# Optimization experiments

Hardware: AMD Instinct MI355X
Metric: run time of the kernel (lower is better)

## Reference

```python
import jax, jax.numpy as jnp
import numpy as np
from jax.ops import segment_sum

N = 20000; IN = 256; HID = 256; Z = 64; DEC_H = 64; E = 120000; NEG = 5
BETA = 1.0; LN_EPS = 1e-5; TAU_MIN = 1e-4


def setup_inputs() -> dict:
    rng = np.random.default_rng(0)
    a = rng.integers(0, N, E)
    b = (a + 1 + rng.integers(0, N - 1, E)) % N  # guarantees a != b
    lo, hi = np.minimum(a, b), np.maximum(a, b)
    pos_edge = jnp.asarray(np.stack([lo, hi]), dtype=jnp.int32)          # [2,E], i<j single copy
    edge_index = jnp.asarray(np.stack([np.concatenate([lo, hi]),
                                       np.concatenate([hi, lo])]), dtype=jnp.int32)  # [2,2E] undirected
    neg_edge = jnp.asarray(rng.integers(0, N, (2, NEG * E)), dtype=jnp.int32)
    ks = jax.random.split(jax.random.key(0), 12)
    p = lambda i, shape, s=0.02: (jax.random.normal(ks[i], shape, jnp.float32) * s)
    return dict(
        x=p(0, (N, IN), 1.0), eps=p(1, (N, Z), 1.0),
        edge_index=edge_index, pos_edge=pos_edge, neg_edge=neg_edge,
        W1=p(2, (IN, HID)), b1=jnp.zeros((HID,), jnp.float32),
        g1=jnp.ones((HID,), jnp.float32), bt1=jnp.zeros((HID,), jnp.float32),
        Wmu=p(3, (HID, Z)), bmu=jnp.zeros((Z,), jnp.float32),
        Wlv=p(4, (HID, Z)), blv=jnp.zeros((Z,), jnp.float32),
        Wd1=p(5, (Z, Z)), bd1=jnp.zeros((Z,), jnp.float32),
        Wd2=p(6, (Z, Z)), bd2=jnp.zeros((Z,), jnp.float32),
        Wa=p(7, (4 * Z, DEC_H)), ba=jnp.zeros((DEC_H,), jnp.float32),
        Wb=p(8, (DEC_H, 1)), bb=jnp.zeros((1,), jnp.float32),
        tau=jnp.array(1.0, jnp.float32))


def _gcn_plain(h, src, dst, W, b):
    # GCNConv(add_self_loops=False, normalize=False): unnormalized scatter-add
    m = h @ W                                   # [N,F]
    return segment_sum(m[src], dst, num_segments=N) + b


def _gcn_norm(h, src, dst, W, b):
    # GCNConv defaults: self loops + symmetric normalization
    loops = jnp.arange(N, dtype=src.dtype)
    s = jnp.concatenate([src, loops]); d = jnp.concatenate([dst, loops])
    deg = segment_sum(jnp.ones_like(d, jnp.float32), d, num_segments=N)  # in-degree incl self
    dis = jax.lax.rsqrt(jnp.maximum(deg, 1.0))
    norm = dis[s] * dis[d]                      # [Emsg+N]
    m = h @ W
    return segment_sum(m[s] * norm[:, None], d, num_segments=N) + b


def _layernorm(h, g, bt):
    mu = jnp.mean(h, axis=-1, keepdims=True)
    var = jnp.mean((h - mu) ** 2, axis=-1, keepdims=True)
    return (h - mu) * jax.lax.rsqrt(var + LN_EPS) * g + bt


def _forward(x, eps, edge_index, pos_edge, neg_edge, W1, b1, g1, bt1, Wmu, bmu,
             Wlv, blv, Wd1, bd1, Wd2, bd2, Wa, ba, Wb, bb, tau):
    src, dst = edge_index[0], edge_index[1]
    # Encoder (dropout inactive: eval-mode reference)
    h1 = jax.nn.relu(_layernorm(_gcn_plain(x, src, dst, W1, b1), g1, bt1))
    mu = _gcn_plain(h1, src, dst, Wmu, bmu)
    logvar = _gcn_plain(h1, src, dst, Wlv, blv)
    z = mu + eps * jnp.exp(0.5 * logvar)
    # EdgeDecoder: 2 normalized GCN passes over positive (i<j) edges only
    ps, pd = pos_edge[0], pos_edge[1]
    h = jax.nn.relu(_gcn_norm(z, ps, pd, Wd1, bd1))
    h = jax.nn.relu(_gcn_norm(h, ps, pd, Wd2, bd2))
    # edge gather -> concat features -> MLP
    eu = jnp.concatenate([pos_edge[0], neg_edge[0]])
    ev = jnp.concatenate([pos_edge[1], neg_edge[1]])
    hu, hv = h[eu], h[ev]                        # [Ep+En, Z]
    phi = jnp.concatenate([hu, hv, jnp.abs(hu - hv), hu * hv], axis=-1)  # [Ep+En, 4Z]
    logits = (jax.nn.relu(phi @ Wa + ba) @ Wb + bb)[:, 0]
    logits = logits / jnp.clip(tau, TAU_MIN)
    # weighted BCE-with-logits; pos_weight = #neg/#pos = NEG
    n_pos = pos_edge.shape[1]; n_neg = neg_edge.shape[1]
    labels = jnp.concatenate([jnp.ones((n_pos,), jnp.float32), jnp.zeros((n_neg,), jnp.float32)])
    pw = jnp.float32(n_neg) / jnp.float32(n_pos)
    recon = -jnp.mean(pw * labels * jax.nn.log_sigmoid(logits)
                      + (1.0 - labels) * jax.nn.log_sigmoid(-logits))
    kl = -0.5 * jnp.mean(1.0 + logvar - mu ** 2 - jnp.exp(logvar))
    loss = recon + BETA * kl
    return loss, recon, kl


def reference(x, eps, edge_index, pos_edge, neg_edge, W1, b1, g1, bt1, Wmu, bmu,
              Wlv, blv, Wd1, bd1, Wd2, bd2, Wa, ba, Wb, bb, tau):
    return _forward(x, eps, edge_index, pos_edge, neg_edge, W1, b1, g1, bt1, Wmu,
                    bmu, Wlv, blv, Wd1, bd1, Wd2, bd2, Wa, ba, Wb, bb, tau)
```

## Files before the change

### kernel.cpp

```cpp
#include <hip/hip_runtime.h>
#include <hip/hip_bf16.h>
#include <math.h>

#define N_NODES 20000
#define E2      240000
#define EP      120000
#define ENEG    600000
#define ETOT    720000
#define NTILE   11250
#define EMLP_BLOCKS 1024

#define WA_B  64
#define W1T_B 256
#define WML_B 128
#define UV_B  2813
#define HA_B  938
#define HP_B  469
#define FA_B  938
#define FP_B  469
#define DIS_B 79

typedef __attribute__((ext_vector_type(8))) short bf16x8;
typedef __attribute__((ext_vector_type(4))) float f32x4;

__device__ __forceinline__ float logsigf(float x) {
    return fminf(x, 0.0f) - log1pf(expf(-fabsf(x)));
}

__device__ __forceinline__ unsigned short f2bf(float f) {
    unsigned u = __float_as_uint(f);
    u += 0x7FFF + ((u >> 16) & 1);
    return (unsigned short)(u >> 16);
}

__device__ __forceinline__ float bflo(unsigned u) { return __uint_as_float(u << 16); }
__device__ __forceinline__ float bfhi(unsigned u) { return __uint_as_float(u & 0xFFFF0000u); }

__device__ __forceinline__ void store_out(float v, float* p) { *p = v; }
__device__ __forceinline__ void store_out(float v, unsigned short* p) { *p = f2bf(v); }
__device__ __forceinline__ float load_in(const float* p) { return *p; }
__device__ __forceinline__ float load_in(const unsigned short* p) {
    return __uint_as_float(((unsigned)*p) << 16);
}

__device__ __forceinline__ int4 pack_phi(unsigned hu, unsigned hv) {
    const float fu0 = __uint_as_float(hu << 16);
    const float fu1 = __uint_as_float(hu & 0xFFFF0000u);
    const float fv0 = __uint_as_float(hv << 16);
    const float fv1 = __uint_as_float(hv & 0xFFFF0000u);
    const float ad0 = fabsf(fu0 - fv0), ad1 = fabsf(fu1 - fv1);
    const float pr0 = fu0 * fv0,        pr1 = fu1 * fv1;
    union { __hip_bfloat162 h; int u; } c0, c1;
    c0.h = __float22bfloat162_rn(float2{ad0, pr0});
    c1.h = __float22bfloat162_rn(float2{ad1, pr1});
    int4 r;
    r.x = (int)((hu & 0xFFFFu) | (hv << 16));
    r.y = c0.u;
    r.z = (int)((hu >> 16) | (hv & 0xFFFF0000u));
    r.w = c1.u;
    return r;
}

__global__ void k_prep_csr(const float* __restrict__ Wa, unsigned short* __restrict__ WaT,
                           const float* __restrict__ W1, unsigned short* __restrict__ W1T,
                           const float* __restrict__ Wmu, const float* __restrict__ Wlv,
                           unsigned short* __restrict__ WmlT,
                           const int* __restrict__ pos, const int* __restrict__ neg,
                           int2* __restrict__ uv,
                           const int* __restrict__ e_dst, int* __restrict__ cntA,
                           const int* __restrict__ pd, int* __restrict__ cntP) {
    const int b = blockIdx.x, tid = threadIdx.x;
    if (b < WA_B) {
        const int idx = b * 256 + tid;
        const int n = idx >> 8, kp = idx & 255;
        const int d = kp >> 2, part = kp & 3;
        WaT[idx] = f2bf(Wa[(part * 64 + d) * 64 + n]);
    } else if (b < WA_B + W1T_B) {
        const int idx = (b - WA_B) * 256 + tid;
        const int n = idx >> 8, k = idx & 255;
        W1T[idx] = f2bf(W1[k * 256 + n]);
    } else if (b < WA_B + W1T_B + WML_B) {
        const int idx = (b - WA_B - W1T_B) * 256 + tid;
        const int n = idx >> 8, k = idx & 255;
        const float* W = (n & 1) ? Wlv : Wmu;
        WmlT[idx] = f2bf(W[k * 64 + (n >> 1)]);
    } else if (b < WA_B + W1T_B + WML_B + UV_B) {
        const int j = (b - WA_B - W1T_B - WML_B) * 256 + tid;
        if (j < ETOT) {
            int u, v;
            if (j < EP) { u = pos[j]; v = pos[EP + j]; }
            else        { u = neg[j - EP]; v = neg[ENEG + (j - EP)]; }
            uv[j] = make_int2(u, v);
        }
    } else if (b < WA_B + W1T_B + WML_B + UV_B + HA_B) {
        const int e = (b - WA_B - W1T_B - WML_B - UV_B) * 256 + tid;
        if (e < E2) atomicAdd(&cntA[e_dst[e]], 1);
    } else {
        const int e = (b - WA_B - W1T_B - WML_B - UV_B - HA_B) * 256 + tid;
        if (e < EP) atomicAdd(&cntP[pd[e]], 1);
    }
}

__global__ __launch_bounds__(1024) void k_scan2(int* __restrict__ cntA, int* __restrict__ rsA,
                                                int* __restrict__ cntP, int* __restrict__ rsP) {
    int* cnt = blockIdx.x ? cntP : cntA;
    int* rs  = blockIdx.x ? rsP  : rsA;
    int* cur = cnt;
    const int n = N_NODES;
    __shared__ int wexc[16];
    __shared__ int s_carry, s_tot;
    const int tid = threadIdx.x, lane = tid & 63, wid = tid >> 6;
    if (tid == 0) s_carry = 0;
    __syncthreads();
    for (int base = 0; base < n; base += 1024) {
        const int i = base + tid;
        const int v = (i < n) ? cnt[i] : 0;
        int x = v;
#pragma unroll
        for (int d = 1; d < 64; d <<= 1) {
            const int t = __shfl_up(x, d, 64);
            if (lane >= d) x += t;
        }
        if (lane == 63) wexc[wid] = x;
        __syncthreads();
        if (tid == 0) {
            int a = 0;
#pragma unroll
            for (int k = 0; k < 16; ++k) { const int t = wexc[k]; wexc[k] = a; a += t; }
            s_tot = a;
        }
        __syncthreads();
        const int excl = s_carry + wexc[wid] + x - v;
        if (i < n) { rs[i] = excl; cur[i] = excl; }
        __syncthreads();
        if (tid == 0) s_carry += s_tot;
        __syncthreads();
    }
    if (tid == 0) rs[n] = s_carry;
}

__global__ void k_finish_csr(const int* __restrict__ e_src, const int* __restrict__ e_dst,
                             int* __restrict__ curA, int* __restrict__ adjA,
                             const int* __restrict__ ps, const int* __restrict__ pd,
                             int* __restrict__ curP, int* __restrict__ adjP,
                             const int* __restrict__ rsP, float* __restrict__ dis) {
    const int b = blockIdx.x, tid = threadIdx.x;
    if (b < FA_B) {
        const int e = b * 256 + tid;
        if (e < E2) {
            const int p = atomicAdd(&curA[e_dst[e]], 1);
            adjA[p] = e_src[e];
        }
    } else if (b < FA_B + FP_B) {
        const int e = (b - FA_B) * 256 + tid;
        if (e < EP) {
            const int p = atomicAdd(&curP[pd[e]], 1);
            adjP[p] = ps[e];
        }
    } else {
        const int i = (b - FA_B - FP_B) * 256 + tid;
        if (i < N_NODES) dis[i] = rsqrtf((float)(rsP[i + 1] - rsP[i] + 1));
    }
}

__global__ __launch_bounds__(256) void k_mm_xW1_mfma(const float* __restrict__ x,
                                                     const unsigned short* __restrict__ W1T,
                                                     unsigned short* __restrict__ m1) {
    __shared__ unsigned short sA[32 * 264];
    const int tid = threadIdx.x;
    const int w = tid >> 6, lane = tid & 63;
    const int l15 = lane & 15, quad = lane >> 4;
    const int mb = blockIdx.x >> 2, nb = blockIdx.x & 3;

    for (int i = tid; i < 2048; i += 256) {
        const int row = i >> 6, kc = (i & 63) << 2;
        const float4 xv = *(const float4*)&x[((long)mb * 32 + row) * 256 + kc];
        union { unsigned short s[4]; unsigned long long ll; } pk;
        pk.s[0] = f2bf(xv.x); pk.s[1] = f2bf(xv.y);
        pk.s[2] = f2bf(xv.z); pk.s[3] = f2bf(xv.w);
        *(unsigned long long*)&sA[row * 264 + kc] = pk.ll;
    }

    bf16x8 breg[8];
#pragma unroll
    for (int ks = 0; ks < 8; ++ks)
        breg[ks] = *(const bf16x8*)&W1T[((nb * 64 + w * 16 + l15) << 8) + ks * 32 + quad * 8];
    __syncthreads();

    f32x4 acc[2];
    acc[0] = (f32x4){0.f,0.f,0.f,0.f};
    acc[1] = (f32x4){0.f,0.f,0.f,0.f};
#pragma unroll
    for (int ks = 0; ks < 8; ++ks) {
#pragma unroll
        for (int st = 0; st < 2; ++st) {
            const bf16x8 af = *(const bf16x8*)&sA[(st * 16 + l15) * 264 + ks * 32 + quad * 8];
            acc[st] = __builtin_amdgcn_mfma_f32_16x16x32_bf16(af, breg[ks], acc[st], 0, 0, 0);
        }
    }
#pragma unroll
    for (int st = 0; st < 2; ++st)
#pragma unroll
        for (int r = 0; r < 4; ++r)
            m1[((long)mb * 32 + st * 16 + quad * 4 + r) * 256 + nb * 64 + w * 16 + l15] =
                f2bf(acc[st][r]);
}

__global__ __launch_bounds__(256) void k_gather_ln(const unsigned short* __restrict__ m1,
                                                   const int* __restrict__ rs,
                                                   const int* __restrict__ adj,
                                                   const float* __restrict__ b1,
                                                   const float* __restrict__ g1,
                                                   const float* __restrict__ bt1,
                                                   unsigned short* __restrict__ h1) {
    const int wid = threadIdx.x >> 6, lane = threadIdx.x & 63;
    const int n = blockIdx.x * 4 + wid;
    const int beg = rs[n], end = rs[n + 1];
    float4 a0 = {0.f,0.f,0.f,0.f}, a1 = {0.f,0.f,0.f,0.f};
    float4 a2 = {0.f,0.f,0.f,0.f}, a3 = {0.f,0.f,0.f,0.f};
    int j = beg;
    for (; j + 3 < end; j += 4) {
        const int s0 = adj[j], s1 = adj[j + 1], s2 = adj[j + 2], s3 = adj[j + 3];
        const uint2 u0 = *(const uint2*)(m1 + (long)s0 * 256 + lane * 4);
        const uint2 u1 = *(const uint2*)(m1 + (long)s1 * 256 + lane * 4);
        const uint2 u2 = *(const uint2*)(m1 + (long)s2 * 256 + lane * 4);
        const uint2 u3 = *(const uint2*)(m1 + (long)s3 * 256 + lane * 4);
        a0.x += bflo(u0.x); a0.y += bfhi(u0.x); a0.z += bflo(u0.y); a0.w += bfhi(u0.y);
        a1.x += bflo(u1.x); a1.y += bfhi(u1.x); a1.z += bflo(u1.y); a1.w += bfhi(u1.y);
        a2.x += bflo(u2.x); a2.y += bfhi(u2.x); a2.z += bflo(u2.y); a2.w += bfhi(u2.y);
        a3.x += bflo(u3.x); a3.y += bfhi(u3.x); a3.z += bflo(u3.y); a3.w += bfhi(u3.y);
    }
    for (; j < end; ++j) {
        const int s0 = adj[j];
        const uint2 u = *(const uint2*)(m1 + (long)s0 * 256 + lane * 4);
        a0.x += bflo(u.x); a0.y += bfhi(u.x); a0.z += bflo(u.y); a0.w += bfhi(u.y);
    }
    float4 v;
    const float4 b = *(const float4*)(b1 + lane * 4);
    v.x = (a0.x + a1.x) + (a2.x + a3.x) + b.x;
    v.y = (a0.y + a1.y) + (a2.y + a3.y) + b.y;
    v.z = (a0.z + a1.z) + (a2.z + a3.z) + b.z;
    v.w = (a0.w + a1.w) + (a2.w + a3.w) + b.w;
    float s  = v.x + v.y + v.z + v.w;
    float sq = v.x * v.x + v.y * v.y + v.z * v.z + v.w * v.w;
    for (int o = 32; o > 0; o >>= 1) {
        s  += __shfl_xor(s, o, 64);
        sq += __shfl_xor(sq, o, 64);
    }
    const float mean = s * (1.0f / 256.0f);
    const float var  = sq * (1.0f / 256.0f) - mean * mean;
    const float rsv = rsqrtf(var + 1e-5f);
    const float4 g  = *(const float4*)(g1 + lane * 4);
    const float4 bt = *(const float4*)(bt1 + lane * 4);
    union { unsigned short sh[4]; unsigned long long ll; } pk;
    pk.sh[0] = f2bf(fmaxf((v.x - mean) * rsv * g.x + bt.x, 0.f));
    pk.sh[1] = f2bf(fmaxf((v.y - mean) * rsv * g.y + bt.y, 0.f));
    pk.sh[2] = f2bf(fmaxf((v.z - mean) * rsv * g.z + bt.z, 0.f));
    pk.sh[3] = f2bf(fmaxf((v.w - mean) * rsv * g.w + bt.w, 0.f));
    *(unsigned long long*)&h1[(long)n * 256 + lane * 4] = pk.ll;
}

__global__ __launch_bounds__(256) void k_mm_hml_mfma(const unsigned short* __restrict__ h1,
                                                     const unsigned short* __restrict__ WmlT,
                                                     unsigned short* __restrict__ hml) {
    __shared__ unsigned short sA[32 * 264];
    const int tid = threadIdx.x;
    const int w = tid >> 6, lane = tid & 63;
    const int l15 = lane & 15, quad = lane >> 4;
    const int mb = blockIdx.x >> 1, nb = blockIdx.x & 1;

    for (int i = tid; i < 1024; i += 256) {
        const int row = i >> 5, kc = (i & 31) << 3;
        *(int4*)&sA[row * 264 + kc] = *(const int4*)&h1[((long)mb * 32 + row) * 256 + kc];
    }

    bf16x8 breg[8];
#pragma unroll
    for (int ks = 0; ks < 8; ++ks)
        breg[ks] = *(const bf16x8*)&WmlT[((nb * 64 + w * 16 + l15) << 8) + ks * 32 + quad * 8];
    __syncthreads();

    f32x4 acc[2];
    acc[0] = (f32x4){0.f,0.f,0.f,0.f};
    acc[1] = (f32x4){0.f,0.f,0.f,0.f};
#pragma unroll
    for (int ks = 0; ks < 8; ++ks) {
#pragma unroll
        for (int st = 0; st < 2; ++st) {
            const bf16x8 af = *(const bf16x8*)&sA[(st * 16 + l15) * 264 + ks * 32 + quad * 8];
            acc[st] = __builtin_amdgcn_mfma_f32_16x16x32_bf16(af, breg[ks], acc[st], 0, 0, 0);
        }
    }
#pragma unroll
    for (int st = 0; st < 2; ++st)
#pragma unroll
        for (int r = 0; r < 4; ++r)
            hml[((long)mb * 32 + st * 16 + quad * 4 + r) * 128 + nb * 64 + w * 16 + l15] =
                f2bf(acc[st][r]);
}

__global__ __launch_bounds__(256) void k_gather_mulv(const unsigned short* __restrict__ hml,
                                                     const int* __restrict__ rs,
                                                     const int* __restrict__ adj,
                                                     const float* __restrict__ bmu,
                                                     const float* __restrict__ blv,
                                                     const float* __restrict__ eps,
                                                     unsigned short* __restrict__ z,
                                                     double* __restrict__ kl_part) {
    __shared__ double sKL[4];
    const int wid = threadIdx.x >> 6, lane = threadIdx.x & 63;
    const int n = blockIdx.x * 4 + wid;
    const int beg = rs[n], end = rs[n + 1];
    float m0 = 0.f, m1_ = 0.f, m2 = 0.f, m3 = 0.f;
    float l0 = 0.f, l1 = 0.f, l2 = 0.f, l3 = 0.f;
    int j = beg;
    for (; j + 3 < end; j += 4) {
        const int s0 = adj[j], s1 = adj[j + 1], s2 = adj[j + 2], s3 = adj[j + 3];
        const unsigned u0 = *(const unsigned*)(hml + (long)s0 * 128 + lane * 2);
        const unsigned u1 = *(const unsigned*)(hml + (long)s1 * 128 + lane * 2);
        const unsigned u2 = *(const unsigned*)(hml + (long)s2 * 128 + lane * 2);
        const unsigned u3 = *(const unsigned*)(hml + (long)s3 * 128 + lane * 2);
        m0 += bflo(u0); l0 += bfhi(u0);
        m1_ += bflo(u1); l1 += bfhi(u1);
        m2 += bflo(u2); l2 += bfhi(u2);
        m3 += bflo(u3); l3 += bfhi(u3);
    }
    for (; j < end; ++j) {
        const int s0 = adj[j];
        const unsigned u0 = *(const unsigned*)(hml + (long)s0 * 128 + lane * 2);
        m0 += bflo(u0); l0 += bfhi(u0);
    }
    const float mu = (m0 + m1_) + (m2 + m3) + bmu[lane];
    const float lv = (l0 + l1) + (l2 + l3) + blv[lane];
    z[(long)n * 64 + lane] = f2bf(mu + eps[(long)n * 64 + lane] * expf(0.5f * lv));
    float term = 1.0f + lv - mu * mu - expf(lv);
    for (int o = 32; o > 0; o >>= 1) term += __shfl_xor(term, o, 64);
    if (lane == 0) sKL[wid] = (double)term;
    __syncthreads();
    if (threadIdx.x == 0)
        kl_part[blockIdx.x] = sKL[0] + sKL[1] + sKL[2] + sKL[3];
}

template <typename IN, typename OUT>
__global__ __launch_bounds__(256) void k_dec_fused(const IN* __restrict__ feat,
                                                   const int* __restrict__ rs,
                                                   const int* __restrict__ adj,
                                                   const float* __restrict__ dis,
                                                   const float* __restrict__ Wd,
                                                   const float* __restrict__ bd,
                                                   OUT* __restrict__ out) {
    __shared__ float sW[64 * 64];
    __shared__ float rows[4][64];
    const int tid = threadIdx.x;
    {
        const float4* w4 = (const float4*)Wd;
        float4* sw4 = (float4*)sW;
        for (int i = tid; i < 1024; i += 256) sw4[i] = w4[i];
    }
    const int wid = tid >> 6, lane = tid & 63;
    const int n = blockIdx.x * 4 + wid;
    const int beg = rs[n], end = rs[n + 1];
    float a0 = 0.f, a1 = 0.f, a2 = 0.f, a3 = 0.f;
    int j = beg;
    for (; j + 3 < end; j += 4) {
        const int s0 = adj[j], s1 = adj[j + 1], s2 = adj[j + 2], s3 = adj[j + 3];
        a0 += load_in(&feat[(long)s0 * 64 + lane]) * dis[s0];
        a1 += load_in(&feat[(long)s1 * 64 + lane]) * dis[s1];
        a2 += load_in(&feat[(long)s2 * 64 + lane]) * dis[s2];
        a3 += load_in(&feat[(long)s3 * 64 + lane]) * dis[s3];
    }
    for (; j < end; ++j) {
        const int s0 = adj[j];
        a0 += load_in(&feat[(long)s0 * 64 + lane]) * dis[s0];
    }
    const float dn = dis[n];
    rows[wid][lane] = ((a0 + a1) + (a2 + a3)) * dn
                    + load_in(&feat[(long)n * 64 + lane]) * dn * dn;
    __syncthreads();
    float acc = 0.f;
    for (int k = 0; k < 64; k += 4) {
        const float4 a = *(const float4*)&rows[wid][k];
        acc += a.x * sW[(k+0)*64+lane] + a.y * sW[(k+1)*64+lane]
             + a.z * sW[(k+2)*64+lane] + a.w * sW[(k+3)*64+lane];
    }
    store_out(fmaxf(acc + bd[lane], 0.f), &out[(long)n * 64 + lane]);
}

__global__ __launch_bounds__(256, 4) void k_edge_mlp_mfma(
        const unsigned short* __restrict__ h2bf,
        const int2* __restrict__ uv,
        const unsigned short* __restrict__ WaT,
        const float* __restrict__ ba,
        const float* __restrict__ Wb,
        const float* __restrict__ bb,
        const float* __restrict__ tau,
        double* __restrict__ recon_part) {
    __shared__ unsigned short sPhi[64 * 264];
    __shared__ float sEp[256];
    __shared__ double sRed[4];
    const int tid = threadIdx.x;
    const int w = tid >> 6, lane = tid & 63;
    const int l15 = lane & 15, quad = lane >> 4;
    const int ge = lane >> 3;
    const int c  = lane & 7;

    bf16x8 breg[8];
#pragma unroll
    for (int ks = 0; ks < 8; ++ks)
        breg[ks] = *(const bf16x8*)&WaT[(w * 16 + l15) * 256 + ks * 32 + quad * 8];

    const float4 ba4 = *(const float4*)&ba[w * 16 + quad * 4];
    const float4 wb4 = *(const float4*)&Wb[w * 16 + quad * 4];
    const float bb0 = bb[0];
    const float itau = 1.0f / fmaxf(tau[0], 1e-4f);

    float lsum = 0.f;

    int t = blockIdx.x;
    int2 uv0 = uv[(long)t * 64 + w * 16 + ge];
    int2 uv1 = uv[(long)t * 64 + w * 16 + 8 + ge];
    int4 hu0 = *(const int4*)&h2bf[(long)uv0.x * 64 + c * 8];
    int4 hv0 = *(const int4*)&h2bf[(long)uv0.y * 64 + c * 8];
    int4 hu1 = *(const int4*)&h2bf[(long)uv1.x * 64 + c * 8];
    int4 hv1 = *(const int4*)&h2bf[(long)uv1.y * 64 + c * 8];

    for (; t < NTILE; t += EMLP_BLOCKS) {
        {
            unsigned short* d0 = &sPhi[(w * 16 + ge) * 264 + c * 32];
            *(int4*)(d0 +  0) = pack_phi((unsigned)hu0.x, (unsigned)hv0.x);
            *(int4*)(d0 +  8) = pack_phi((unsigned)hu0.y, (unsigned)hv0.y);
            *(int4*)(d0 + 16) = pack_phi((unsigned)hu0.z, (unsigned)hv0.z);
            *(int4*)(d0 + 24) = pack_phi((unsigned)hu0.w, (unsigned)hv0.w);
            unsigned short* d1 = &sPhi[(w * 16 + 8 + ge) * 264 + c * 32];
            *(int4*)(d1 +  0) = pack_phi((unsigned)hu1.x, (unsigned)hv1.x);
            *(int4*)(d1 +  8) = pack_phi((unsigned)hu1.y, (unsigned)hv1.y);
            *(int4*)(d1 + 16) = pack_phi((unsigned)hu1.z, (unsigned)hv1.z);
            *(int4*)(d1 + 24) = pack_phi((unsigned)hu1.w, (unsigned)hv1.w);
        }
        __syncthreads();

        const int tn = t + EMLP_BLOCKS;
        if (tn < NTILE) {
            uv0 = uv[(long)tn * 64 + w * 16 + ge];
            uv1 = uv[(long)tn * 64 + w * 16 + 8 + ge];
            hu0 = *(const int4*)&h2bf[(long)uv0.x * 64 + c * 8];
            hv0 = *(const int4*)&h2bf[(long)uv0.y * 64 + c * 8];
            hu1 = *(const int4*)&h2bf[(long)uv1.x * 64 + c * 8];
            hv1 = *(const int4*)&h2bf[(long)uv1.y * 64 + c * 8];
        }

        f32x4 acc[4];
#pragma unroll
        for (int mt = 0; mt < 4; ++mt) acc[mt] = (f32x4){0.f, 0.f, 0.f, 0.f};
#pragma unroll
        for (int ks = 0; ks < 8; ++ks) {
#pragma unroll
            for (int mt = 0; mt < 4; ++mt) {
                const bf16x8 bf = *(const bf16x8*)&sPhi[(mt * 16 + l15) * 264 +
                                                        ks * 32 + quad * 8];
                acc[mt] = __builtin_amdgcn_mfma_f32_16x16x32_bf16(breg[ks], bf, acc[mt], 0, 0, 0);
            }
        }

        float sv[4];
#pragma unroll
        for (int mt = 0; mt < 4; ++mt) {
            float s = fmaxf(acc[mt][0] + ba4.x, 0.f) * wb4.x
                    + fmaxf(acc[mt][1] + ba4.y, 0.f) * wb4.y
                    + fmaxf(acc[mt][2] + ba4.z, 0.f) * wb4.z
                    + fmaxf(acc[mt][3] + ba4.w, 0.f) * wb4.w;
            s += __shfl_xor(s, 16, 64);
            s += __shfl_xor(s, 32, 64);
            sv[mt] = s;
        }
        const float ssel = (quad == 0) ? sv[0] : (quad == 1) ? sv[1]
                         : (quad == 2) ? sv[2] : sv[3];
        sEp[(w << 6) + lane] = ssel;
        __syncthreads();

        if (lane < 16) {
            const int et = (w << 4) + lane;
            const float s_e = sEp[et] + sEp[64 + et] + sEp[128 + et] + sEp[192 + et];
            const long j = (long)t * 64 + et;
            const float logit = (s_e + bb0) * itau;
            lsum += (j < EP) ? 5.0f * logsigf(logit) : logsigf(-logit);
        }
    }

    for (int o = 32; o > 0; o >>= 1) lsum += __shfl_xor(lsum, o, 64);
    if (lane == 0) sRed[w] = (double)lsum;
    __syncthreads();
    if (tid == 0)
        recon_part[blockIdx.x] = sRed[0] + sRed[1] + sRed[2] + sRed[3];
}

__global__ __launch_bounds__(1024) void k_final(const double* __restrict__ kl_part,
                                                const double* __restrict__ recon_part,
                                                float* __restrict__ out) {
    __shared__ double sK[16], sR[16];
    const int tid = threadIdx.x, lane = tid & 63, wid = tid >> 6;
    double kl = 0.0, rc = 0.0;
    for (int i = tid; i < 5000; i += 1024) kl += kl_part[i];
    for (int i = tid; i < EMLP_BLOCKS; i += 1024) rc += recon_part[i];
    for (int o = 32; o > 0; o >>= 1) {
        kl += __shfl_xor(kl, o, 64);
        rc += __shfl_xor(rc, o, 64);
    }
    if (lane == 0) { sK[wid] = kl; sR[wid] = rc; }
    __syncthreads();
    if (tid == 0) {
        double K = 0.0, R = 0.0;
        for (int i = 0; i < 16; ++i) { K += sK[i]; R += sR[i]; }
        const double recon = -R / (double)ETOT;
        const double klv = -0.5 * K / ((double)N_NODES * 64.0);
        out[0] = (float)(recon + klv);
        out[1] = (float)recon;
        out[2] = (float)klv;
    }
}

extern "C" void kernel_launch(void* const* d_in, const int* in_sizes, int n_in,
                              void* d_out, int out_size, void* d_ws, size_t ws_size,
                              hipStream_t stream) {
    const float* x   = (const float*)d_in[0];
    const float* eps = (const float*)d_in[1];
    const int* EI    = (const int*)d_in[2];
    const int* pos   = (const int*)d_in[3];
    const int* neg   = (const int*)d_in[4];
    const float* W1  = (const float*)d_in[5];
    const float* b1  = (const float*)d_in[6];
    const float* g1  = (const float*)d_in[7];
    const float* bt1 = (const float*)d_in[8];
    const float* Wmu = (const float*)d_in[9];
    const float* bmu = (const float*)d_in[10];
    const float* Wlv = (const float*)d_in[11];
    const float* blv = (const float*)d_in[12];
    const float* Wd1 = (const float*)d_in[13];
    const float* bd1 = (const float*)d_in[14];
    const float* Wd2 = (const float*)d_in[15];
    const float* bd2 = (const float*)d_in[16];
    const float* Wa  = (const float*)d_in[17];
    const float* ba  = (const float*)d_in[18];
    const float* Wb  = (const float*)d_in[19];
    const float* bb  = (const float*)d_in[20];
    const float* tau = (const float*)d_in[21];

    const int* e_src = EI;
    const int* e_dst = EI + E2;
    const int* ps = pos;
    const int* pd = pos + EP;

    float* ws = (float*)d_ws;
    unsigned short* m1bf  = (unsigned short*)ws;
    unsigned short* hmlbf = (unsigned short*)ws;
    unsigned short* hdec  = (unsigned short*)(ws + 2560000);
    unsigned short* h2bf = (unsigned short*)(ws + 3840000);
    unsigned short* h1bf = (unsigned short*)(ws + 5120000);
    unsigned short* z    = (unsigned short*)(ws + 10240000);
    float* dis   = ws + 11520000;
    unsigned short* WaT = (unsigned short*)(ws + 11540004);
    int* cntA = (int*)(ws + 11548200);
    int* rsA  = (int*)(ws + 11568200);
    int* adjA = (int*)(ws + 11588204);
    int* cntP = (int*)(ws + 11828204);
    int* rsP  = (int*)(ws + 11848204);
    int* adjP = (int*)(ws + 11868208);
    int2* uv  = (int2*)(ws + 11988208);
    double* kl_part    = (double*)(ws + 13428208);
    double* recon_part = (double*)(ws + 13438208);
    unsigned short* W1T  = (unsigned short*)(ws + 13440256);
    unsigned short* WmlT = (unsigned short*)(ws + 13473024);

    hipMemsetAsync(cntA, 0, N_NODES * 4, stream);
    hipMemsetAsync(cntP, 0, N_NODES * 4, stream);

    k_prep_csr<<<WA_B + W1T_B + WML_B + UV_B + HA_B + HP_B, 256, 0, stream>>>(
        Wa, WaT, W1, W1T, Wmu, Wlv, WmlT, pos, neg, uv, e_dst, cntA, pd, cntP);
    k_scan2<<<2, 1024, 0, stream>>>(cntA, rsA, cntP, rsP);
    k_finish_csr<<<FA_B + FP_B + DIS_B, 256, 0, stream>>>(
        e_src, e_dst, cntA, adjA, ps, pd, cntP, adjP, rsP, dis);

    k_mm_xW1_mfma<<<2500, 256, 0, stream>>>(x, W1T, m1bf);
    k_gather_ln<<<5000, 256, 0, stream>>>(m1bf, rsA, adjA, b1, g1, bt1, h1bf);
    k_mm_hml_mfma<<<1250, 256, 0, stream>>>(h1bf, WmlT, hmlbf);
    k_gather_mulv<<<5000, 256, 0, stream>>>(hmlbf, rsA, adjA, bmu, blv, eps, z, kl_part);

    k_dec_fused<unsigned short, unsigned short><<<5000, 256, 0, stream>>>(
        z, rsP, adjP, dis, Wd1, bd1, hdec);
    k_dec_fused<unsigned short, unsigned short><<<5000, 256, 0, stream>>>(
        hdec, rsP, adjP, dis, Wd2, bd2, h2bf);

    k_edge_mlp_mfma<<<EMLP_BLOCKS, 256, 0, stream>>>(h2bf, uv, WaT, ba, Wb, bb, tau, recon_part);
    k_final<<<1, 1024, 0, stream>>>(kl_part, recon_part, (float*)d_out);
}
```

Baseline: 338.8 us.

## Build edge-MLP MFMA operands in registers, dropping the LDS phi staging and block barriers

The edge MLP kernel no longer writes the phi feature tile to shared memory. Each wave now gathers its 16 edges' hu/hv rows directly into MFMA B-operand registers, computes |hu-hv| and hu*hv in registers, and keeps the whole WaT weight matrix (all four N-tiles) resident as A-operands. The WaT prep permutes the K ordering to match this register layout. Each wave computes all 64 hidden outputs for its own edges, so the two __syncthreads per tile and the cross-wave sEp reduction go away. In exchange register pressure rises (32 bf16x8 weight registers per lane), so launch_bounds drops to 2 blocks per SM, which may reduce latency hiding for the gathers.

```diff
diff --git a/kernel.cpp b/kernel.cpp
--- a/kernel.cpp
+++ b/kernel.cpp
@@ -43,22 +43,34 @@
     return __uint_as_float(((unsigned)*p) << 16);
 }
 
-__device__ __forceinline__ int4 pack_phi(unsigned hu, unsigned hv) {
-    const float fu0 = __uint_as_float(hu << 16);
-    const float fu1 = __uint_as_float(hu & 0xFFFF0000u);
-    const float fv0 = __uint_as_float(hv << 16);
-    const float fv1 = __uint_as_float(hv & 0xFFFF0000u);
-    const float ad0 = fabsf(fu0 - fv0), ad1 = fabsf(fu1 - fv1);
-    const float pr0 = fu0 * fv0,        pr1 = fu1 * fv1;
-    union { __hip_bfloat162 h; int u; } c0, c1;
-    c0.h = __float22bfloat162_rn(float2{ad0, pr0});
-    c1.h = __float22bfloat162_rn(float2{ad1, pr1});
-    int4 r;
-    r.x = (int)((hu & 0xFFFFu) | (hv << 16));
-    r.y = c0.u;
-    r.z = (int)((hu >> 16) | (hv & 0xFFFF0000u));
-    r.w = c1.u;
-    return r;
+__device__ __forceinline__ bf16x8 make_ad(int4 a, int4 b) {
+    const unsigned* pa = (const unsigned*)&a;
+    const unsigned* pb = (const unsigned*)&b;
+    union { unsigned u[4]; bf16x8 v; } out;
+#pragma unroll
+    for (int i = 0; i < 4; ++i) {
+        const float lo = fabsf(bflo(pa[i]) - bflo(pb[i]));
+        const float hi = fabsf(bfhi(pa[i]) - bfhi(pb[i]));
+        union { __hip_bfloat162 h; unsigned u; } c;
+        c.h = __float22bfloat162_rn(float2{lo, hi});
+        out.u[i] = c.u;
+    }
+    return out.v;
+}
+
+__device__ __forceinline__ bf16x8 make_pr(int4 a, int4 b) {
+    const unsigned* pa = (const unsigned*)&a;
+    const unsigned* pb = (const unsigned*)&b;
+    union { unsigned u[4]; bf16x8 v; } out;
+#pragma unroll
+    for (int i = 0; i < 4; ++i) {
+        const float lo = bflo(pa[i]) * bflo(pb[i]);
+        const float hi = bfhi(pa[i]) * bfhi(pb[i]);
+        union { __hip_bfloat162 h; unsigned u; } c;
+        c.h = __float22bfloat162_rn(float2{lo, hi});
+        out.u[i] = c.u;
+    }
+    return out.v;
 }
 
 __global__ void k_prep_csr(const float* __restrict__ Wa, unsigned short* __restrict__ WaT,
@@ -73,7 +85,8 @@
     if (b < WA_B) {
         const int idx = b * 256 + tid;
         const int n = idx >> 8, kp = idx & 255;
-        const int d = kp >> 2, part = kp & 3;
+        const int part = kp >> 6;
+        const int d = ((kp >> 3) & 3) * 16 + ((kp >> 5) & 1) * 8 + (kp & 7);
         WaT[idx] = f2bf(Wa[(part * 64 + d) * 64 + n]);
     } else if (b < WA_B + W1T_B) {
         const int idx = (b - WA_B) * 256 + tid;
@@ -386,7 +399,7 @@
     store_out(fmaxf(acc + bd[lane], 0.f), &out[(long)n * 64 + lane]);
 }
 
-__global__ __launch_bounds__(256, 4) void k_edge_mlp_mfma(
+__global__ __launch_bounds__(256, 2) void k_edge_mlp_mfma(
         const unsigned short* __restrict__ h2bf,
         const int2* __restrict__ uv,
         const unsigned short* __restrict__ WaT,
@@ -395,94 +408,84 @@
         const float* __restrict__ bb,
         const float* __restrict__ tau,
         double* __restrict__ recon_part) {
-    __shared__ unsigned short sPhi[64 * 264];
-    __shared__ float sEp[256];
     __shared__ double sRed[4];
     const int tid = threadIdx.x;
     const int w = tid >> 6, lane = tid & 63;
     const int l15 = lane & 15, quad = lane >> 4;
-    const int ge = lane >> 3;
-    const int c  = lane & 7;
-
-    bf16x8 breg[8];
-#pragma unroll
-    for (int ks = 0; ks < 8; ++ks)
-        breg[ks] = *(const bf16x8*)&WaT[(w * 16 + l15) * 256 + ks * 32 + quad * 8];
-
-    const float4 ba4 = *(const float4*)&ba[w * 16 + quad * 4];
-    const float4 wb4 = *(const float4*)&Wb[w * 16 + quad * 4];
+
+    bf16x8 areg[4][8];
+#pragma unroll
+    for (int nt = 0; nt < 4; ++nt)
+#pragma unroll
+        for (int ks = 0; ks < 8; ++ks)
+            areg[nt][ks] = *(const bf16x8*)&WaT[((nt * 16 + l15) << 8) + ks * 32 + quad * 8];
+
     const float bb0 = bb[0];
     const float itau = 1.0f / fmaxf(tau[0], 1e-4f);
 
     float lsum = 0.f;
 
     int t = blockIdx.x;
-    int2 uv0 = uv[(long)t * 64 + w * 16 + ge];
-    int2 uv1 = uv[(long)t * 64 + w * 16 + 8 + ge];
-    int4 hu0 = *(const int4*)&h2bf[(long)uv0.x * 64 + c * 8];
-    int4 hv0 = *(const int4*)&h2bf[(long)uv0.y * 64 + c * 8];
-    int4 hu1 = *(const int4*)&h2bf[(long)uv1.x * 64 + c * 8];
-    int4 hv1 = *(const int4*)&h2bf[(long)uv1.y * 64 + c * 8];
+    int2 uvp = uv[t * 64 + w * 16 + l15];
+    int4 hua = *(const int4*)&h2bf[uvp.x * 64 + quad * 16];
+    int4 hub = *(const int4*)&h2bf[uvp.x * 64 + quad * 16 + 8];
+    int4 hva = *(const int4*)&h2bf[uvp.y * 64 + quad * 16];
+    int4 hvb = *(const int4*)&h2bf[uvp.y * 64 + quad * 16 + 8];
 
     for (; t < NTILE; t += EMLP_BLOCKS) {
-        {
-            unsigned short* d0 = &sPhi[(w * 16 + ge) * 264 + c * 32];
-            *(int4*)(d0 +  0) = pack_phi((unsigned)hu0.x, (unsigned)hv0.x);
-            *(int4*)(d0 +  8) = pack_phi((unsigned)hu0.y, (unsigned)hv0.y);
-            *(int4*)(d0 + 16) = pack_phi((unsigned)hu0.z, (unsigned)hv0.z);
-            *(int4*)(d0 + 24) = pack_phi((unsigned)hu0.w, (unsigned)hv0.w);
-            unsigned short* d1 = &sPhi[(w * 16 + 8 + ge) * 264 + c * 32];
-            *(int4*)(d1 +  0) = pack_phi((unsigned)hu1.x, (unsigned)hv1.x);
-            *(int4*)(d1 +  8) = pack_phi((unsigned)hu1.y, (unsigned)hv1.y);
-            *(int4*)(d1 + 16) = pack_phi((unsigned)hu1.z, (unsigned)hv1.z);
-            *(int4*)(d1 + 24) = pack_phi((unsigned)hu1.w, (unsigned)hv1.w);
-        }
-        __syncthreads();
-
         const int tn = t + EMLP_BLOCKS;
+        int2 uvn = uvp;
+        if (tn < NTILE) uvn = uv[tn * 64 + w * 16 + l15];
+
+        const bf16x8 fad_a = make_ad(hua, hva);
+        const bf16x8 fad_b = make_ad(hub, hvb);
+        const bf16x8 fpr_a = make_pr(hua, hva);
+        const bf16x8 fpr_b = make_pr(hub, hvb);
+
+        f32x4 acc[4];
+#pragma unroll
+        for (int nt = 0; nt < 4; ++nt) acc[nt] = (f32x4){0.f, 0.f, 0.f, 0.f};
+
+        const bf16x8 bhu_a = *(const bf16x8*)&hua;
+        const bf16x8 bhu_b = *(const bf16x8*)&hub;
+        const bf16x8 bhv_a = *(const bf16x8*)&hva;
+        const bf16x8 bhv_b = *(const bf16x8*)&hvb;
+
+#pragma unroll
+        for (int nt = 0; nt < 4; ++nt) {
+            acc[nt] = __builtin_amdgcn_mfma_f32_16x16x32_bf16(areg[nt][0], bhu_a, acc[nt], 0, 0, 0);
+            acc[nt] = __builtin_amdgcn_mfma_f32_16x16x32_bf16(areg[nt][1], bhu_b, acc[nt], 0, 0, 0);
+            acc[nt] = __builtin_amdgcn_mfma_f32_16x16x32_bf16(areg[nt][2], bhv_a, acc[nt], 0, 0, 0);
+            acc[nt] = __builtin_amdgcn_mfma_f32_16x16x32_bf16(areg[nt][3], bhv_b, acc[nt], 0, 0, 0);
+            acc[nt] = __builtin_amdgcn_mfma_f32_16x16x32_bf16(areg[nt][4], fad_a, acc[nt], 0, 0, 0);
+            acc[nt] = __builtin_amdgcn_mfma_f32_16x16x32_bf16(areg[nt][5], fad_b, acc[nt], 0, 0, 0);
+            acc[nt] = __builtin_amdgcn_mfma_f32_16x16x32_bf16(areg[nt][6], fpr_a, acc[nt], 0, 0, 0);
+            acc[nt] = __builtin_amdgcn_mfma_f32_16x16x32_bf16(areg[nt][7], fpr_b, acc[nt], 0, 0, 0);
+        }
+
         if (tn < NTILE) {
-            uv0 = uv[(long)tn * 64 + w * 16 + ge];
-            uv1 = uv[(long)tn * 64 + w * 16 + 8 + ge];
-            hu0 = *(const int4*)&h2bf[(long)uv0.x * 64 + c * 8];
-            hv0 = *(const int4*)&h2bf[(long)uv0.y * 64 + c * 8];
-            hu1 = *(const int4*)&h2bf[(long)uv1.x * 64 + c * 8];
-            hv1 = *(const int4*)&h2bf[(long)uv1.y * 64 + c * 8];
-        }
-
-        f32x4 acc[4];
-#pragma unroll
-        for (int mt = 0; mt < 4; ++mt) acc[mt] = (f32x4){0.f, 0.f, 0.f, 0.f};
-#pragma unroll
-        for (int ks = 0; ks < 8; ++ks) {
-#pragma unroll
-            for (int mt = 0; mt < 4; ++mt) {
-                const bf16x8 bf = *(const bf16x8*)&sPhi[(mt * 16 + l15) * 264 +
-                                                        ks * 32 + quad * 8];
-                acc[mt] = __builtin_amdgcn_mfma_f32_16x16x32_bf16(breg[ks], bf, acc[mt], 0, 0, 0);
-            }
-        }
-
-        float sv[4];
-#pragma unroll
-        for (int mt = 0; mt < 4; ++mt) {
-            float s = fmaxf(acc[mt][0] + ba4.x, 0.f) * wb4.x
-                    + fmaxf(acc[mt][1] + ba4.y, 0.f) * wb4.y
-                    + fmaxf(acc[mt][2] + ba4.z, 0.f) * wb4.z
-                    + fmaxf(acc[mt][3] + ba4.w, 0.f) * wb4.w;
-            s += __shfl_xor(s, 16, 64);
-            s += __shfl_xor(s, 32, 64);
-            sv[mt] = s;
-        }
-        const float ssel = (quad == 0) ? sv[0] : (quad == 1) ? sv[1]
-                         : (quad == 2) ? sv[2] : sv[3];
-        sEp[(w << 6) + lane] = ssel;
-        __syncthreads();
-
+            hua = *(const int4*)&h2bf[uvn.x * 64 + quad * 16];
+            hub = *(const int4*)&h2bf[uvn.x * 64 + quad * 16 + 8];
+            hva = *(const int4*)&h2bf[uvn.y * 64 + quad * 16];
+            hvb = *(const int4*)&h2bf[uvn.y * 64 + quad * 16 + 8];
+        }
+        uvp = uvn;
+
+        float s = 0.f;
+#pragma unroll
+        for (int nt = 0; nt < 4; ++nt) {
+            const float4 b4 = *(const float4*)&ba[nt * 16 + quad * 4];
+            const float4 w4 = *(const float4*)&Wb[nt * 16 + quad * 4];
+            s += fmaxf(acc[nt][0] + b4.x, 0.f) * w4.x
+               + fmaxf(acc[nt][1] + b4.y, 0.f) * w4.y
+               + fmaxf(acc[nt][2] + b4.z, 0.f) * w4.z
+               + fmaxf(acc[nt][3] + b4.w, 0.f) * w4.w;
+        }
+        s += __shfl_xor(s, 16, 64);
+        s += __shfl_xor(s, 32, 64);
         if (lane < 16) {
-            const int et = (w << 4) + lane;
-            const float s_e = sEp[et] + sEp[64 + et] + sEp[128 + et] + sEp[192 + et];
-            const long j = (long)t * 64 + et;
-            const float logit = (s_e + bb0) * itau;
+            const long j = (long)t * 64 + w * 16 + lane;
+            const float logit = (s + bb0) * itau;
             lsum += (j < EP) ? 5.0f * logsigf(logit) : logsigf(-logit);
         }
     }
```

Measured after the change: 333.9 us. About the same (-1.4%).
